# Optimization experiments

Measured on AMD Instinct MI355X. Metric: run time of the kernel, lower is better.

Reference implementation:

```python
import jax, jax.numpy as jnp
import numpy as np
import math

KEY_DIM = 16
COMPAT_FACTOR = 1.0 / math.sqrt(KEY_DIM)


def setup_inputs() -> dict:
    key = jax.random.key(0)
    k1, k2, k3, k4, k5 = jax.random.split(key, 5)
    B, G, D, H, K, V = 4, 2048, 128, 8, 16, 16
    h = jax.random.normal(k1, (B, G, D), dtype=jnp.float32)
    # mask: 1 = masked-out (attention forced to zero), 0 = attend
    mask = jax.random.randint(k2, (G, G), 0, 2, dtype=jnp.int32)
    # xavier_uniform over (input_dim, key_dim) fan per head
    lim_qk = math.sqrt(6.0 / (D + K))
    lim_v = math.sqrt(6.0 / (D + V))
    W_Q = jax.random.uniform(k3, (H, D, K), jnp.float32, -lim_qk, lim_qk)
    W_K = jax.random.uniform(k4, (H, D, K), jnp.float32, -lim_qk, lim_qk)
    W_V = jax.random.uniform(k5, (H, D, V), jnp.float32, -lim_v, lim_v)
    return {"h": h, "mask": mask, "W_Q": W_Q, "W_K": W_K, "W_V": W_V}


def reference(h, mask, W_Q, W_K, W_V):
    # h: [B, G, D]; W_Q/W_K: [H, D, K]; W_V: [H, D, V]; mask: [G, G] (1 = masked)
    q = jnp.einsum("bgd,hdk->bhgk", h, W_Q)  # [B, H, G, K]
    k = jnp.einsum("bgd,hdk->bhgk", h, W_K)  # [B, H, G, K]
    v = jnp.einsum("bgd,hdv->bhgv", h, W_V)  # [B, H, G, V]
    compat = COMPAT_FACTOR * jnp.einsum("bhqk,bhgk->bhqg", q, k)  # [B, H, G, G]
    masked = (mask > 0)[None, None, :, :]  # broadcast over batch, heads
    neg = jnp.finfo(compat.dtype).min
    compat = jnp.where(masked, neg, compat)
    attn = jax.nn.softmax(compat, axis=-1)
    # post-softmax hard zeroing at masked positions (as in the original)
    attn = jnp.where(masked, jnp.zeros((), attn.dtype), attn)
    h_p = jnp.einsum("bhqg,bhgv->bhqv", attn, v)  # [B, H, G, V]
    return h_p
```

## Files before the change

### kernel.cpp

```cpp
#include <hip/hip_runtime.h>
#include <hip/hip_bf16.h>

#define GG 2048
#define DD 128
#define HH 8
#define BH 32

typedef _Float16 h2 __attribute__((ext_vector_type(2)));
typedef _Float16 h4 __attribute__((ext_vector_type(4)));
typedef _Float16 h8 __attribute__((ext_vector_type(8)));
typedef __attribute__((ext_vector_type(4))) float f32x4;
typedef unsigned short u16;
typedef unsigned int   u32;
typedef unsigned char  u8;
typedef unsigned long long u64;

#define QSCALE 0.36067376022224085f

#define OFF_Q  0u
#define OFF_KV (2u << 20)
#define OFF_M  (6u << 20)

#if __has_builtin(__builtin_amdgcn_exp2f)
#define EXP2F(x) __builtin_amdgcn_exp2f(x)
#else
#define EXP2F(x) exp2f(x)
#endif

#define MFMA16(a, b, c) __builtin_amdgcn_mfma_f32_16x16x16f16(a, b, c, 0, 0, 0)

static __device__ __forceinline__ u16 f16b(float x) {
  return __builtin_bit_cast(u16, (_Float16)x);
}

__global__ __launch_bounds__(256) void prep_kernel(
    const float* __restrict__ h, const int* __restrict__ mask,
    const float* __restrict__ WQ, const float* __restrict__ WK,
    const float* __restrict__ WV,
    _Float16* __restrict__ Qh, u8* __restrict__ KVp, u8* __restrict__ mbt)
{
  const int blk = blockIdx.x, tid = threadIdx.x;

  if (blk >= 256) {
    int t = (blk - 256) * 256 + tid;
    const int* m = mask + (size_t)t * 8;
    int4 m0 = *(const int4*)m;
    int4 m1 = *(const int4*)(m + 4);
    u32 byte = (m0.x > 0) | ((m0.y > 0) << 1) | ((m0.z > 0) << 2) | ((m0.w > 0) << 3)
             | ((m1.x > 0) << 4) | ((m1.y > 0) << 5) | ((m1.z > 0) << 6) | ((m1.w > 0) << 7);
    int q  = t >> 8;
    int k8 = t & 255;
    mbt[(size_t)(k8 >> 4) * (GG * 16) + (size_t)q * 16 + (k8 & 15)] = (u8)byte;
    return;
  }

  __shared__ _Float16 Wl[48 * 136];
  const int bh = blk >> 3, b = bh >> 3, hh = bh & (HH - 1);

  #pragma unroll
  for (int m = 0; m < 3; ++m) {
    const float* W = (m == 0 ? WQ : (m == 1 ? WK : WV)) + (size_t)hh * DD * 16;
    const float sc = (m == 0) ? QSCALE : 1.0f;
    #pragma unroll
    for (int i = 0; i < 2; ++i) {
      int j4 = i * 256 + tid;
      float4 v = ((const float4*)W)[j4];
      int j = j4 * 4, d = j >> 4, n0 = m * 16 + (j & 15);
      Wl[(n0 + 0) * 136 + d] = (_Float16)(v.x * sc);
      Wl[(n0 + 1) * 136 + d] = (_Float16)(v.y * sc);
      Wl[(n0 + 2) * 136 + d] = (_Float16)(v.z * sc);
      Wl[(n0 + 3) * 136 + d] = (_Float16)(v.w * sc);
    }
  }
  __syncthreads();

  const int wave = tid >> 6, lane = tid & 63;
  const int col = lane & 15, quad = lane >> 4;
  const int g0 = ((blk & 7) * 4 + wave) * 64;
  const float* hb = h + (size_t)b * GG * DD;

  f32x4 acc[4][3];
  #pragma unroll
  for (int mt = 0; mt < 4; ++mt)
    #pragma unroll
    for (int nt = 0; nt < 3; ++nt)
      acc[mt][nt] = (f32x4){0.f, 0.f, 0.f, 0.f};

  #pragma unroll
  for (int s = 0; s < 4; ++s) {
    h8 a[4], bw[3];
    #pragma unroll
    for (int mt = 0; mt < 4; ++mt) {
      const float* src = hb + (size_t)(g0 + mt * 16 + col) * DD + s * 32 + quad * 8;
      float4 x = ((const float4*)src)[0];
      float4 y = ((const float4*)src)[1];
      a[mt] = (h8){ (_Float16)x.x, (_Float16)x.y, (_Float16)x.z, (_Float16)x.w,
                    (_Float16)y.x, (_Float16)y.y, (_Float16)y.z, (_Float16)y.w };
    }
    #pragma unroll
    for (int nt = 0; nt < 3; ++nt)
      bw[nt] = *(const h8*)&Wl[(nt * 16 + col) * 136 + s * 32 + quad * 8];
    #pragma unroll
    for (int mt = 0; mt < 4; ++mt)
      #pragma unroll
      for (int nt = 0; nt < 3; ++nt)
        acc[mt][nt] = __builtin_amdgcn_mfma_f32_16x16x32_f16(a[mt], bw[nt], acc[mt][nt], 0, 0, 0);
  }

  u8* kvb = KVp + (size_t)bh * 16 * 8192;
  #pragma unroll
  for (int mt = 0; mt < 4; ++mt) {
    #pragma unroll
    for (int r = 0; r < 4; ++r) {
      int g = g0 + mt * 16 + quad * 4 + r;
      Qh[((size_t)bh * GG + g) * 16 + col] = (_Float16)acc[mt][0][r];
      int gi = g & 127;
      u8* tb = kvb + (size_t)(g >> 7) * 8192;
      *(u16*)(tb + gi * 32 + col * 2) = f16b(acc[mt][1][r]);
      *(u16*)(tb + 4096 + col * 256 + ((((gi >> 2) + col) & 31) * 8)
                 + (g & 3) * 2) = f16b(acc[mt][2][r]);
    }
  }
}

__global__ __launch_bounds__(256, 4) void attn_kernel(
    const _Float16* __restrict__ Qh, const u8* __restrict__ KVp,
    const u8* __restrict__ mbt, float* __restrict__ out)
{
  __shared__ __align__(16) u8 kv[2][8192];
  const int tid = threadIdx.x, wv = tid >> 6, lane = tid & 63;
  const int col = lane & 15, quad = lane >> 4;
  const int bh = blockIdx.x & 31;
  const int qb = (blockIdx.x >> 5) * 64 + wv * 16;

  const h4 qf = *(const h4*)(Qh + ((size_t)bh * GG + qb + col) * 16 + quad * 4);
  const u8* kvsrc = KVp + (size_t)bh * 16 * 8192;
  const u8* mrow  = mbt + (size_t)(qb + col) * 16;

  {
    uint4 p0 = *(const uint4*)(kvsrc + tid * 32);
    uint4 p1 = *(const uint4*)(kvsrc + tid * 32 + 16);
    *(uint4*)(kv[0] + tid * 32) = p0;
    *(uint4*)(kv[0] + tid * 32 + 16) = p1;
  }
  uint4 mv = *(const uint4*)mrow;
  __syncthreads();

  f32x4 acc = {0.f,0.f,0.f,0.f}, lacc = {0.f,0.f,0.f,0.f};
  const f32x4 cinit = {-4.f, -4.f, -4.f, -4.f};
  const h4 ones = {(_Float16)1.f, (_Float16)1.f, (_Float16)1.f, (_Float16)1.f};

  for (int kt = 0; kt < 16; ++kt) {
    uint4 ns0, ns1, nmv;
    if (kt < 15) {
      const u8* nsrc = kvsrc + (size_t)(kt + 1) * 8192 + tid * 32;
      ns0 = *(const uint4*)nsrc;
      ns1 = *(const uint4*)(nsrc + 16);
      nmv = *(const uint4*)(mrow + (size_t)(kt + 1) * (GG * 16));
    }

    const u8* cur = kv[kt & 1];
    const _Float16* ldsK = (const _Float16*)cur;
    const u8* ldsV = cur + 4096;
    u64 w0 = (u64)mv.x | ((u64)mv.y << 32);
    u64 w1 = (u64)mv.z | ((u64)mv.w << 32);

    #pragma unroll
    for (int st = 0; st < 8; ++st) {
      h4 kf = *(const h4*)(ldsK + (size_t)(st * 16 + col) * 16 + quad * 4);
      h4 vf = *(const h4*)(ldsV + col * 256 + (((st * 4 + quad + col) & 31) * 8));

      f32x4 s = MFMA16(kf, qf, cinit);
      const int sh = (st & 3) * 16 + quad * 4;
      u32 bits = (u32)(((st < 4) ? w0 : w1) >> sh) & 0xFu;
      float p0 = (bits & 1u) ? 0.f : EXP2F(s[0]);
      float p1 = (bits & 2u) ? 0.f : EXP2F(s[1]);
      float p2 = (bits & 4u) ? 0.f : EXP2F(s[2]);
      float p3 = (bits & 8u) ? 0.f : EXP2F(s[3]);

      h2 a01 = __builtin_bit_cast(h2, __builtin_amdgcn_cvt_pkrtz(p0, p1));
      h2 a23 = __builtin_bit_cast(h2, __builtin_amdgcn_cvt_pkrtz(p2, p3));
      h4 pf = __builtin_shufflevector(a01, a23, 0, 1, 2, 3);

      acc  = MFMA16(vf, pf, acc);
      lacc = MFMA16(ones, pf, lacc);
    }

    if (kt < 15) {
      u8* nb = kv[(kt + 1) & 1];
      *(uint4*)(nb + tid * 32) = ns0;
      *(uint4*)(nb + tid * 32 + 16) = ns1;
      mv = nmv;
      __syncthreads();
    }
  }

  const float l = lacc[0];
  const float rl = (l > 0.f) ? (1.f / l) : 0.f;
  float4 o = { acc[0] * rl, acc[1] * rl, acc[2] * rl, acc[3] * rl };
  *(float4*)(out + ((size_t)bh * GG + qb + col) * 16 + quad * 4) = o;
}

extern "C" void kernel_launch(void* const* d_in, const int* in_sizes, int n_in,
                              void* d_out, int out_size, void* d_ws, size_t ws_size,
                              hipStream_t stream) {
  const float* h    = (const float*)d_in[0];
  const int*   mask = (const int*)d_in[1];
  const float* WQ   = (const float*)d_in[2];
  const float* WK   = (const float*)d_in[3];
  const float* WV   = (const float*)d_in[4];
  float* out = (float*)d_out;
  char* ws = (char*)d_ws;
  _Float16* Qh  = (_Float16*)(ws + OFF_Q);
  u8*       KVp = (u8*)(ws + OFF_KV);
  u8*       mbt = (u8*)(ws + OFF_M);

  hipLaunchKernelGGL(prep_kernel, dim3(256 + GG * GG / (256 * 8)), dim3(256), 0, stream,
                     h, mask, WQ, WK, WV, Qh, KVp, mbt);
  hipLaunchKernelGGL(attn_kernel, dim3(BH * (GG / 64)), dim3(256), 0, stream,
                     Qh, KVp, mbt, out);
}
```

Baseline: 112.2 us.

## Double attention block size and process two K/V tiles per barrier

The attention kernel now uses 512-thread blocks covering 128 queries instead of 64, so each K/V tile staged in LDS is shared by twice as many waves. Two 128-key tiles are loaded together per iteration, which halves the number of __syncthreads barriers and global-to-LDS staging rounds. The mask word shift by quad is also hoisted out of the inner loop. In exchange, LDS use per block doubles to 32 KB, the grid has half as many blocks (512), and larger blocks may lower scheduling flexibility or occupancy.

```diff
diff --git a/kernel.cpp b/kernel.cpp
--- a/kernel.cpp
+++ b/kernel.cpp
@@ -123,56 +123,37 @@
   }
 }
 
-__global__ __launch_bounds__(256, 4) void attn_kernel(
+__global__ __launch_bounds__(512, 4) void attn_kernel(
     const _Float16* __restrict__ Qh, const u8* __restrict__ KVp,
     const u8* __restrict__ mbt, float* __restrict__ out)
 {
-  __shared__ __align__(16) u8 kv[2][8192];
+  __shared__ __align__(16) u8 kv[2][16384];
   const int tid = threadIdx.x, wv = tid >> 6, lane = tid & 63;
   const int col = lane & 15, quad = lane >> 4;
   const int bh = blockIdx.x & 31;
-  const int qb = (blockIdx.x >> 5) * 64 + wv * 16;
+  const int qb = (blockIdx.x >> 5) * 128 + wv * 16;
 
   const h4 qf = *(const h4*)(Qh + ((size_t)bh * GG + qb + col) * 16 + quad * 4);
   const u8* kvsrc = KVp + (size_t)bh * 16 * 8192;
   const u8* mrow  = mbt + (size_t)(qb + col) * 16;
 
-  {
-    uint4 p0 = *(const uint4*)(kvsrc + tid * 32);
-    uint4 p1 = *(const uint4*)(kvsrc + tid * 32 + 16);
-    *(uint4*)(kv[0] + tid * 32) = p0;
-    *(uint4*)(kv[0] + tid * 32 + 16) = p1;
-  }
-  uint4 mv = *(const uint4*)mrow;
-  __syncthreads();
-
   f32x4 acc = {0.f,0.f,0.f,0.f}, lacc = {0.f,0.f,0.f,0.f};
   const f32x4 cinit = {-4.f, -4.f, -4.f, -4.f};
   const h4 ones = {(_Float16)1.f, (_Float16)1.f, (_Float16)1.f, (_Float16)1.f};
-
-  for (int kt = 0; kt < 16; ++kt) {
-    uint4 ns0, ns1, nmv;
-    if (kt < 15) {
-      const u8* nsrc = kvsrc + (size_t)(kt + 1) * 8192 + tid * 32;
-      ns0 = *(const uint4*)nsrc;
-      ns1 = *(const uint4*)(nsrc + 16);
-      nmv = *(const uint4*)(mrow + (size_t)(kt + 1) * (GG * 16));
-    }
-
-    const u8* cur = kv[kt & 1];
+  const int shq = quad * 4;
+
+  auto tile = [&](const u8* cur, uint4 mv) {
     const _Float16* ldsK = (const _Float16*)cur;
     const u8* ldsV = cur + 4096;
-    u64 w0 = (u64)mv.x | ((u64)mv.y << 32);
-    u64 w1 = (u64)mv.z | ((u64)mv.w << 32);
-
+    u64 w0 = ((u64)mv.x | ((u64)mv.y << 32)) >> shq;
+    u64 w1 = ((u64)mv.z | ((u64)mv.w << 32)) >> shq;
     #pragma unroll
     for (int st = 0; st < 8; ++st) {
       h4 kf = *(const h4*)(ldsK + (size_t)(st * 16 + col) * 16 + quad * 4);
       h4 vf = *(const h4*)(ldsV + col * 256 + (((st * 4 + quad + col) & 31) * 8));
 
       f32x4 s = MFMA16(kf, qf, cinit);
-      const int sh = (st & 3) * 16 + quad * 4;
-      u32 bits = (u32)(((st < 4) ? w0 : w1) >> sh) & 0xFu;
+      u32 bits = (u32)(((st < 4) ? w0 : w1) >> ((st & 3) * 16)) & 0xFu;
       float p0 = (bits & 1u) ? 0.f : EXP2F(s[0]);
       float p1 = (bits & 2u) ? 0.f : EXP2F(s[1]);
       float p2 = (bits & 4u) ? 0.f : EXP2F(s[2]);
@@ -185,12 +166,37 @@
       acc  = MFMA16(vf, pf, acc);
       lacc = MFMA16(ones, pf, lacc);
     }
-
-    if (kt < 15) {
-      u8* nb = kv[(kt + 1) & 1];
-      *(uint4*)(nb + tid * 32) = ns0;
-      *(uint4*)(nb + tid * 32 + 16) = ns1;
-      mv = nmv;
+  };
+
+  {
+    uint4 a0 = *(const uint4*)(kvsrc + tid * 32);
+    uint4 a1 = *(const uint4*)(kvsrc + tid * 32 + 16);
+    *(uint4*)(kv[0] + tid * 32) = a0;
+    *(uint4*)(kv[0] + tid * 32 + 16) = a1;
+  }
+  uint4 mv0 = *(const uint4*)mrow;
+  uint4 mv1 = *(const uint4*)(mrow + (size_t)(GG * 16));
+  __syncthreads();
+
+  for (int it = 0; it < 8; ++it) {
+    uint4 na0, na1, nm0, nm1;
+    if (it < 7) {
+      const u8* ns = kvsrc + (size_t)(it + 1) * 16384 + tid * 32;
+      na0 = *(const uint4*)ns;
+      na1 = *(const uint4*)(ns + 16);
+      nm0 = *(const uint4*)(mrow + (size_t)(2 * it + 2) * (GG * 16));
+      nm1 = *(const uint4*)(mrow + (size_t)(2 * it + 3) * (GG * 16));
+    }
+
+    const u8* cur = kv[it & 1];
+    tile(cur, mv0);
+    tile(cur + 8192, mv1);
+
+    if (it < 7) {
+      u8* nb = kv[(it + 1) & 1];
+      *(uint4*)(nb + tid * 32) = na0;
+      *(uint4*)(nb + tid * 32 + 16) = na1;
+      mv0 = nm0; mv1 = nm1;
       __syncthreads();
     }
   }
@@ -217,6 +223,6 @@
 
   hipLaunchKernelGGL(prep_kernel, dim3(256 + GG * GG / (256 * 8)), dim3(256), 0, stream,
                      h, mask, WQ, WK, WV, Qh, KVp, mbt);
-  hipLaunchKernelGGL(attn_kernel, dim3(BH * (GG / 64)), dim3(256), 0, stream,
+  hipLaunchKernelGGL(attn_kernel, dim3(BH * (GG / 128)), dim3(512), 0, stream,
                      Qh, KVp, mbt, out);
 }
```

Result: no change. 112.6 us (+0.4%).
